# Optimization experiments

Measured on AMD Instinct MI355X. Metric: run time of the kernel, lower is better.

The kernel has to match this reference:

```python
import jax, jax.numpy as jnp
import numpy as np

NF = 256  # node_feat_size
GF = 256  # graph_feat_size
V = 262144
G = 4096


def setup_inputs() -> dict:
    key = jax.random.key(0)
    ks = jax.random.split(key, 12)
    node_feats = jax.random.normal(ks[0], (V, NF), dtype=jnp.float32)
    g_feats = jax.random.normal(ks[1], (G, GF), dtype=jnp.float32)
    segment_ids = jnp.sort(jax.random.randint(ks[2], (V,), 0, G, dtype=jnp.int32))
    s = 0.05
    # compute_logits: Linear(NF+GF -> 1)
    Wl = jax.random.normal(ks[3], (1, NF + GF), dtype=jnp.float32) * s
    bl = jnp.zeros((1,), dtype=jnp.float32)
    # project_nodes: Linear(NF -> GF)  (dropout=0 -> identity)
    Wp = jax.random.normal(ks[4], (GF, NF), dtype=jnp.float32) * s
    bp = jnp.zeros((GF,), dtype=jnp.float32)
    # GRUCell(GF, GF), torch gate order (r, z, n)
    W_ih = jax.random.normal(ks[5], (3 * GF, GF), dtype=jnp.float32) * s
    W_hh = jax.random.normal(ks[6], (3 * GF, GF), dtype=jnp.float32) * s
    b_ih = jnp.zeros((3 * GF,), dtype=jnp.float32)
    b_hh = jnp.zeros((3 * GF,), dtype=jnp.float32)
    return dict(node_feats=node_feats, g_feats=g_feats, segment_ids=segment_ids,
                Wl=Wl, bl=bl, Wp=Wp, bp=bp,
                W_ih=W_ih, W_hh=W_hh, b_ih=b_ih, b_hh=b_hh)


def reference(node_feats, g_feats, segment_ids, Wl, bl, Wp, bp, W_ih, W_hh, b_ih, b_hh):
    num_graphs = g_feats.shape[0]
    # broadcast relu(g_feats) to nodes, concat with node feats, logits Linear + LeakyReLU
    gb = jax.nn.relu(g_feats)[segment_ids]                      # [V, GF]
    cat = jnp.concatenate([gb, node_feats], axis=1)             # [V, GF+NF]
    z = jax.nn.leaky_relu(cat @ Wl.T + bl, negative_slope=0.01) # [V, 1]
    # segmented softmax over nodes per graph
    m = jax.ops.segment_max(z, segment_ids, num_segments=num_graphs,
                            indices_are_sorted=True)            # [G, 1]
    e = jnp.exp(z - m[segment_ids])                             # [V, 1]
    denom = jax.ops.segment_sum(e, segment_ids, num_segments=num_graphs,
                                indices_are_sorted=True)        # [G, 1]
    a = e / denom[segment_ids]                                  # [V, 1]
    # project nodes (dropout p=0 -> identity) and weighted sum per graph
    hv = node_feats @ Wp.T + bp                                 # [V, GF]
    context = jax.ops.segment_sum(a * hv, segment_ids, num_segments=num_graphs,
                                  indices_are_sorted=True)      # [G, GF]
    context = jax.nn.elu(context)
    # GRUCell: input=context, hidden=g_feats, torch gate order r,z,n
    gi = context @ W_ih.T + b_ih                                # [G, 3*GF]
    gh = g_feats @ W_hh.T + b_hh                                # [G, 3*GF]
    i_r, i_z, i_n = jnp.split(gi, 3, axis=1)
    h_r, h_z, h_n = jnp.split(gh, 3, axis=1)
    r = jax.nn.sigmoid(i_r + h_r)
    u = jax.nn.sigmoid(i_z + h_z)
    n = jnp.tanh(i_n + r * h_n)
    h_new = (1.0 - u) * n + u * g_feats
    return h_new
```

## Files before the change

### kernel.cpp

```cpp
#include <hip/hip_runtime.h>
#include <hip/hip_bf16.h>
#include <stdint.h>

typedef unsigned short u16;
typedef __attribute__((ext_vector_type(8))) short short8;
typedef __attribute__((ext_vector_type(4))) float floatx4;

#define NFEAT 256

__device__ __forceinline__ unsigned short f2b(float f) {
    unsigned int x = __builtin_bit_cast(unsigned int, f);
    x += 0x7fffu + ((x >> 16) & 1u);
    return (unsigned short)(x >> 16);
}
__device__ __forceinline__ float sigmoidf_(float x) {
    return 1.0f / (1.0f + __expf(-x));
}

__global__ void __launch_bounds__(256)
k1_attn_pool(const float* __restrict__ nf, const float* __restrict__ gf,
             const int* __restrict__ seg, const float* __restrict__ Wl,
             const float* __restrict__ bl,
             const float* __restrict__ Wp, const float* __restrict__ Wih,
             const float* __restrict__ Whh,
             u16* __restrict__ s_out,
             float* __restrict__ pres, u16* __restrict__ gfb,
             u16* __restrict__ wpb, u16* __restrict__ wihb, u16* __restrict__ whhb,
             int V)
{
    const int g = blockIdx.x;
    const int t = threadIdx.x;
    __shared__ float red[256];
    __shared__ float accs[4][256];
    __shared__ float lws[4];

    {
        const int n1 = 256 * 256;
        const int n2 = n1 + 768 * 256;
        const int n3 = n2 + 768 * 256;
        int idx = g * 256 + t;
        if (idx < n3) {
            if (idx < n1)       wpb[idx]       = f2b(Wp[idx]);
            else if (idx < n2)  wihb[idx - n1] = f2b(Wih[idx - n1]);
            else                whhb[idx - n2] = f2b(Whh[idx - n2]);
        }
    }

    const float gfv = gf[(size_t)g * NFEAT + t];
    gfb[(size_t)g * NFEAT + t] = f2b(gfv);
    red[t] = fmaxf(gfv, 0.0f) * Wl[t];
    __syncthreads();
    #pragma unroll
    for (int off = 128; off > 0; off >>= 1) {
        if (t < off) red[t] += red[t + off];
        __syncthreads();
    }
    const float gbase = red[0] + bl[0];
    __syncthreads();

    int lo = 0, hi = V;
    while (lo < hi) { int mid = (lo + hi) >> 1; if (seg[mid] < g) lo = mid + 1; else hi = mid; }
    const int start = lo;
    hi = V;
    while (lo < hi) { int mid = (lo + hi) >> 1; if (seg[mid] <= g) lo = mid + 1; else hi = mid; }
    const int count = lo - start;

    const int lane = t & 63;
    const int wv = t >> 6;

    const float4 wn = *(const float4*)(Wl + NFEAT + lane * 4);

    float l = 0.0f;
    float4 acc = {0.f, 0.f, 0.f, 0.f};
    const float* base = nf + (size_t)start * NFEAT + lane * 4;

    float4 x[4] = {{0,0,0,0},{0,0,0,0},{0,0,0,0},{0,0,0,0}};
    #pragma unroll
    for (int r = 0; r < 4; ++r) {
        int i = wv * 4 + r;
        if (i < count) x[r] = *(const float4*)(base + (size_t)i * NFEAT);
    }
    for (int i = wv * 4; i < count; i += 16) {
        float4 nx[4] = {{0,0,0,0},{0,0,0,0},{0,0,0,0},{0,0,0,0}};
        #pragma unroll
        for (int r = 0; r < 4; ++r) {
            if (i + 16 + r < count) nx[r] = *(const float4*)(base + (size_t)(i + 16 + r) * NFEAT);
        }
        float d[4];
        #pragma unroll
        for (int r = 0; r < 4; ++r)
            d[r] = x[r].x * wn.x + x[r].y * wn.y + x[r].z * wn.z + x[r].w * wn.w;
        #pragma unroll
        for (int off = 32; off > 0; off >>= 1) {
            #pragma unroll
            for (int r = 0; r < 4; ++r) d[r] += __shfl_xor(d[r], off);
        }
        #pragma unroll
        for (int r = 0; r < 4; ++r) {
            float z = d[r] + gbase;
            z = (z > 0.0f) ? z : 0.01f * z;
            float p = (i + r < count) ? __expf(z) : 0.0f;
            l += p;
            acc.x += p * x[r].x;
            acc.y += p * x[r].y;
            acc.z += p * x[r].z;
            acc.w += p * x[r].w;
        }
        x[0] = nx[0]; x[1] = nx[1]; x[2] = nx[2]; x[3] = nx[3];
    }

    accs[wv][lane * 4 + 0] = acc.x;
    accs[wv][lane * 4 + 1] = acc.y;
    accs[wv][lane * 4 + 2] = acc.z;
    accs[wv][lane * 4 + 3] = acc.w;
    if (lane == 0) lws[wv] = l;
    __syncthreads();

    const float L = (lws[0] + lws[1]) + (lws[2] + lws[3]);
    const float sv = (accs[0][t] + accs[1][t]) + (accs[2][t] + accs[3][t]);
    const float inv = (L > 0.0f) ? 1.0f / L : 0.0f;
    s_out[(size_t)g * NFEAT + t] = f2b(sv * inv);
    if (t == 0) pres[g] = (count > 0) ? 1.0f : 0.0f;
}

#define CTX_LD 264
__global__ void __launch_bounds__(512)
k2_fused(const u16* __restrict__ s, const u16* __restrict__ wpb,
         const float* __restrict__ bp, const float* __restrict__ pres,
         const u16* __restrict__ gfb, const float* __restrict__ gf,
         const u16* __restrict__ wihb, const u16* __restrict__ whhb,
         const float* __restrict__ bih, const float* __restrict__ bhh,
         float* __restrict__ out)
{
    __shared__ u16 ctx[16][CTX_LD];
    const int t = threadIdx.x;
    const int w = t >> 6;
    const int lane = t & 63;
    const int m0 = blockIdx.x * 16;
    const int lr = lane & 15;
    const int kh = lane >> 4;

    {
        const short* A = (const short*)s + (size_t)(m0 + lr) * NFEAT + kh * 8;
        short8 af[8];
        #pragma unroll
        for (int kk = 0; kk < 8; ++kk) af[kk] = *(const short8*)(A + kk * 32);

        #pragma unroll
        for (int nt = 0; nt < 2; ++nt) {
            const int n0 = (w * 2 + nt) * 16;
            const short* B = (const short*)wpb + (size_t)(n0 + lr) * NFEAT + kh * 8;
            floatx4 acc = {0.f, 0.f, 0.f, 0.f};
            #pragma unroll
            for (int kk = 0; kk < 8; ++kk)
                acc = __builtin_amdgcn_mfma_f32_16x16x32_bf16(af[kk], *(const short8*)(B + kk * 32), acc, 0, 0, 0);
            const int col = n0 + lr;
            const float bias = bp[col];
            #pragma unroll
            for (int r = 0; r < 4; ++r) {
                int rl = kh * 4 + r;
                float x = acc[r] + bias * pres[m0 + rl];
                x = (x > 0.0f) ? x : (__expf(x) - 1.0f);
                ctx[rl][col] = f2b(x);
            }
        }
    }
    __syncthreads();

    short8 a1[8], a2[8];
    #pragma unroll
    for (int kk = 0; kk < 8; ++kk)
        a1[kk] = *(const short8*)&ctx[lr][kk * 32 + kh * 8];
    {
        const short* A2 = (const short*)gfb + (size_t)(m0 + lr) * NFEAT + kh * 8;
        #pragma unroll
        for (int kk = 0; kk < 8; ++kk) a2[kk] = *(const short8*)(A2 + kk * 32);
    }

    #pragma unroll
    for (int jt = 0; jt < 2; ++jt) {
        const int j0 = (w * 2 + jt) * 16;
        const size_t boff = (size_t)(j0 + lr) * NFEAT + kh * 8;
        const short* Bir = (const short*)wihb + boff;
        const short* Biz = Bir + 256 * NFEAT;
        const short* Bin = Bir + 512 * NFEAT;
        const short* Bhr = (const short*)whhb + boff;
        const short* Bhz = Bhr + 256 * NFEAT;
        const short* Bhn = Bhr + 512 * NFEAT;

        floatx4 air = {0,0,0,0}, aiz = {0,0,0,0}, ain = {0,0,0,0};
        floatx4 ahr = {0,0,0,0}, ahz = {0,0,0,0}, ahn = {0,0,0,0};
        #pragma unroll
        for (int kk = 0; kk < 8; ++kk) {
            const int k = kk * 32;
            air = __builtin_amdgcn_mfma_f32_16x16x32_bf16(a1[kk], *(const short8*)(Bir + k), air, 0, 0, 0);
            aiz = __builtin_amdgcn_mfma_f32_16x16x32_bf16(a1[kk], *(const short8*)(Biz + k), aiz, 0, 0, 0);
            ain = __builtin_amdgcn_mfma_f32_16x16x32_bf16(a1[kk], *(const short8*)(Bin + k), ain, 0, 0, 0);
            ahr = __builtin_amdgcn_mfma_f32_16x16x32_bf16(a2[kk], *(const short8*)(Bhr + k), ahr, 0, 0, 0);
            ahz = __builtin_amdgcn_mfma_f32_16x16x32_bf16(a2[kk], *(const short8*)(Bhz + k), ahz, 0, 0, 0);
            ahn = __builtin_amdgcn_mfma_f32_16x16x32_bf16(a2[kk], *(const short8*)(Bhn + k), ahn, 0, 0, 0);
        }
        const int col = j0 + lr;
        const float b_ir = bih[col], b_iz = bih[256 + col], b_in = bih[512 + col];
        const float b_hr = bhh[col], b_hz = bhh[256 + col], b_hn = bhh[512 + col];
        #pragma unroll
        for (int r = 0; r < 4; ++r) {
            int row = m0 + kh * 4 + r;
            float rg = sigmoidf_((air[r] + b_ir) + (ahr[r] + b_hr));
            float ug = sigmoidf_((aiz[r] + b_iz) + (ahz[r] + b_hz));
            float ng = tanhf((ain[r] + b_in) + rg * (ahn[r] + b_hn));
            float h  = gf[(size_t)row * NFEAT + col];
            out[(size_t)row * NFEAT + col] = (1.0f - ug) * ng + ug * h;
        }
    }
}

extern "C" void kernel_launch(void* const* d_in, const int* in_sizes, int n_in,
                              void* d_out, int out_size, void* d_ws, size_t ws_size,
                              hipStream_t stream)
{
    const float* nf  = (const float*)d_in[0];
    const float* gf  = (const float*)d_in[1];
    const int*   seg = (const int*)d_in[2];
    const float* Wl  = (const float*)d_in[3];
    const float* bl  = (const float*)d_in[4];
    const float* Wp  = (const float*)d_in[5];
    const float* bp  = (const float*)d_in[6];
    const float* Wih = (const float*)d_in[7];
    const float* Whh = (const float*)d_in[8];
    const float* bih = (const float*)d_in[9];
    const float* bhh = (const float*)d_in[10];

    const int V = in_sizes[2];
    const int G = in_sizes[1] / NFEAT;

    char* ws = (char*)d_ws;
    u16*   sbuf = (u16*)ws;                           ws += (size_t)G * NFEAT * 2;
    u16*   gfb  = (u16*)ws;                           ws += (size_t)G * NFEAT * 2;
    u16*   wpb  = (u16*)ws;                           ws += (size_t)256 * 256 * 2;
    u16*   wihb = (u16*)ws;                           ws += (size_t)768 * 256 * 2;
    u16*   whhb = (u16*)ws;                           ws += (size_t)768 * 256 * 2;
    float* pres = (float*)ws;                         ws += (size_t)G * 4;

    k1_attn_pool<<<G, 256, 0, stream>>>(nf, gf, seg, Wl, bl, Wp, Wih, Whh,
                                        sbuf, pres, gfb, wpb, wihb, whhb, V);
    k2_fused<<<G / 16, 512, 0, stream>>>(sbuf, wpb, bp, pres, gfb, gf,
                                         wihb, whhb, bih, bhh, (float*)d_out);
    (void)ws_size; (void)n_in; (void)out_size;
}
```

Measured before the change: 428.4 us.

## Precompute segment offsets in prep kernel and move weight conversion out of pooling kernel

Adds a prep kernel that builds per-graph start offsets from the sorted segment ids and converts the weight matrices to bf16 two elements per thread. The pooling kernel no longer runs two binary searches per block and no longer carries the weight conversion. It also swaps the shared-memory tree reduction for a wave-shuffle reduction and issues the first node loads before computing the graph bias. The cost is one extra kernel launch and an offsets buffer in the workspace.

```diff
diff --git a/kernel.cpp b/kernel.cpp
--- a/kernel.cpp
+++ b/kernel.cpp
@@ -18,68 +18,80 @@
 }
 
 __global__ void __launch_bounds__(256)
-k1_attn_pool(const float* __restrict__ nf, const float* __restrict__ gf,
-             const int* __restrict__ seg, const float* __restrict__ Wl,
-             const float* __restrict__ bl,
-             const float* __restrict__ Wp, const float* __restrict__ Wih,
-             const float* __restrict__ Whh,
-             u16* __restrict__ s_out,
-             float* __restrict__ pres, u16* __restrict__ gfb,
-             u16* __restrict__ wpb, u16* __restrict__ wihb, u16* __restrict__ whhb,
-             int V)
-{
-    const int g = blockIdx.x;
-    const int t = threadIdx.x;
-    __shared__ float red[256];
-    __shared__ float accs[4][256];
-    __shared__ float lws[4];
+k0_prep(const int* __restrict__ seg, int V, int G, int* __restrict__ off,
+        const float* __restrict__ Wp, const float* __restrict__ Wih,
+        const float* __restrict__ Whh,
+        u16* __restrict__ wpb, u16* __restrict__ wihb, u16* __restrict__ whhb)
+{
+    const int i = blockIdx.x * 256 + threadIdx.x;
 
     {
         const int n1 = 256 * 256;
         const int n2 = n1 + 768 * 256;
         const int n3 = n2 + 768 * 256;
-        int idx = g * 256 + t;
+        int idx = i * 2;
         if (idx < n3) {
-            if (idx < n1)       wpb[idx]       = f2b(Wp[idx]);
-            else if (idx < n2)  wihb[idx - n1] = f2b(Wih[idx - n1]);
-            else                whhb[idx - n2] = f2b(Whh[idx - n2]);
-        }
-    }
-
-    const float gfv = gf[(size_t)g * NFEAT + t];
-    gfb[(size_t)g * NFEAT + t] = f2b(gfv);
-    red[t] = fmaxf(gfv, 0.0f) * Wl[t];
-    __syncthreads();
-    #pragma unroll
-    for (int off = 128; off > 0; off >>= 1) {
-        if (t < off) red[t] += red[t + off];
-        __syncthreads();
-    }
-    const float gbase = red[0] + bl[0];
-    __syncthreads();
-
-    int lo = 0, hi = V;
-    while (lo < hi) { int mid = (lo + hi) >> 1; if (seg[mid] < g) lo = mid + 1; else hi = mid; }
-    const int start = lo;
-    hi = V;
-    while (lo < hi) { int mid = (lo + hi) >> 1; if (seg[mid] <= g) lo = mid + 1; else hi = mid; }
-    const int count = lo - start;
-
+            const float* src; u16* dst; int o;
+            if (idx < n1)      { src = Wp;  dst = wpb;  o = idx; }
+            else if (idx < n2) { src = Wih; dst = wihb; o = idx - n1; }
+            else               { src = Whh; dst = whhb; o = idx - n2; }
+            float2 v = *(const float2*)(src + o);
+            dst[o]     = f2b(v.x);
+            dst[o + 1] = f2b(v.y);
+        }
+    }
+
+    if (i < V) {
+        int s = seg[i];
+        int prev = (i == 0) ? -1 : seg[i - 1];
+        if (s != prev) {
+            for (int g2 = prev + 1; g2 <= s; ++g2) off[g2] = i;
+        }
+        if (i == V - 1) {
+            for (int g2 = s + 1; g2 <= G; ++g2) off[g2] = V;
+        }
+    }
+}
+
+__global__ void __launch_bounds__(256)
+k1_attn_pool(const float* __restrict__ nf, const float* __restrict__ gf,
+             const int* __restrict__ off, const float* __restrict__ Wl,
+             const float* __restrict__ bl,
+             u16* __restrict__ s_out,
+             float* __restrict__ pres, u16* __restrict__ gfb)
+{
+    const int g = blockIdx.x;
+    const int t = threadIdx.x;
     const int lane = t & 63;
     const int wv = t >> 6;
-
-    const float4 wn = *(const float4*)(Wl + NFEAT + lane * 4);
-
-    float l = 0.0f;
-    float4 acc = {0.f, 0.f, 0.f, 0.f};
+    __shared__ float red[4];
+    __shared__ float accs[4][256];
+    __shared__ float lws[4];
+
+    const int start = off[g];
+    const int count = off[g + 1] - start;
+
     const float* base = nf + (size_t)start * NFEAT + lane * 4;
-
     float4 x[4] = {{0,0,0,0},{0,0,0,0},{0,0,0,0},{0,0,0,0}};
     #pragma unroll
     for (int r = 0; r < 4; ++r) {
         int i = wv * 4 + r;
         if (i < count) x[r] = *(const float4*)(base + (size_t)i * NFEAT);
     }
+
+    const float4 wn = *(const float4*)(Wl + NFEAT + lane * 4);
+
+    const float gfv = gf[(size_t)g * NFEAT + t];
+    gfb[(size_t)g * NFEAT + t] = f2b(gfv);
+    float v = fmaxf(gfv, 0.0f) * Wl[t];
+    #pragma unroll
+    for (int o = 32; o > 0; o >>= 1) v += __shfl_xor(v, o);
+    if (lane == 0) red[wv] = v;
+    __syncthreads();
+    const float gbase = (red[0] + red[1]) + (red[2] + red[3]) + bl[0];
+
+    float l = 0.0f;
+    float4 acc = {0.f, 0.f, 0.f, 0.f};
     for (int i = wv * 4; i < count; i += 16) {
         float4 nx[4] = {{0,0,0,0},{0,0,0,0},{0,0,0,0},{0,0,0,0}};
         #pragma unroll
@@ -91,9 +103,9 @@
         for (int r = 0; r < 4; ++r)
             d[r] = x[r].x * wn.x + x[r].y * wn.y + x[r].z * wn.z + x[r].w * wn.w;
         #pragma unroll
-        for (int off = 32; off > 0; off >>= 1) {
+        for (int o = 32; o > 0; o >>= 1) {
             #pragma unroll
-            for (int r = 0; r < 4; ++r) d[r] += __shfl_xor(d[r], off);
+            for (int r = 0; r < 4; ++r) d[r] += __shfl_xor(d[r], o);
         }
         #pragma unroll
         for (int r = 0; r < 4; ++r) {
@@ -241,9 +253,11 @@
     u16*   wihb = (u16*)ws;                           ws += (size_t)768 * 256 * 2;
     u16*   whhb = (u16*)ws;                           ws += (size_t)768 * 256 * 2;
     float* pres = (float*)ws;                         ws += (size_t)G * 4;
-
-    k1_attn_pool<<<G, 256, 0, stream>>>(nf, gf, seg, Wl, bl, Wp, Wih, Whh,
-                                        sbuf, pres, gfb, wpb, wihb, whhb, V);
+    int*   off  = (int*)ws;                           ws += (size_t)(G + 1) * 4;
+
+    k0_prep<<<(V + 255) / 256, 256, 0, stream>>>(seg, V, G, off, Wp, Wih, Whh,
+                                                 wpb, wihb, whhb);
+    k1_attn_pool<<<G, 256, 0, stream>>>(nf, gf, off, Wl, bl, sbuf, pres, gfb);
     k2_fused<<<G / 16, 512, 0, stream>>>(sbuf, wpb, bp, pres, gfb, gf,
                                          wihb, whhb, bih, bhh, (float*)d_out);
     (void)ws_size; (void)n_in; (void)out_size;
```

Measured after the change: 420.4 us. Within noise of the previous version (-1.8%).
